# Kernel optimization log

Measured on AMD Instinct MI355X. Metric: run time of the kernel, lower is better.

## Reference

```python
import jax, jax.numpy as jnp
import numpy as np

NC = 32          # num context requests
NG = 32          # num generation requests
L = 4            # max_draft_len
CTX_LEN = 512    # tokens per context request
NCTX_TOK = NC * CTX_LEN            # 16384
NTOK = NCTX_TOK + NG * (L + 1)     # 16544
H = 2048
NCAP = 3                            # captured layers
VT = 50257                          # target vocab
VD = 32000                          # draft vocab


def setup_inputs() -> dict:
    key = jax.random.key(0)
    ks = jax.random.split(key, 10)
    logits = jax.random.normal(ks[0], (NC + NG * (L + 1), VT), jnp.float32)
    input_ids = jax.random.randint(ks[1], (NTOK,), 0, VT, jnp.int32)
    position_ids = jnp.arange(NTOK, dtype=jnp.int32)
    captured_hidden = jax.random.normal(ks[2], (NTOK, NCAP * H), jnp.float32)
    draft_tokens = jax.random.randint(ks[3], (NG * L,), 0, VT, jnp.int32)
    # last token index of each context request
    gather_ids_ctx = (jnp.arange(1, NC + 1, dtype=jnp.int32) * CTX_LEN - 1)
    s = 1.0 / np.sqrt(H)
    W_fc = jax.random.normal(ks[4], (NCAP * H, H), jnp.float32) * s
    embed = jax.random.normal(ks[5], (VT, H), jnp.float32) * s
    W_h = jax.random.normal(ks[6], (H, H), jnp.float32) * s
    lm_head = jax.random.normal(ks[7], (H, VD), jnp.float32) * s
    d2t = jax.random.randint(ks[8], (VD,), 0, VT - VD, jnp.int32)
    return {
        'logits': logits, 'input_ids': input_ids, 'position_ids': position_ids,
        'captured_hidden': captured_hidden, 'draft_tokens': draft_tokens,
        'gather_ids_ctx': gather_ids_ctx, 'W_fc': W_fc, 'embed': embed,
        'W_h': W_h, 'lm_head': lm_head, 'd2t': d2t,
        'num_contexts': NC, 'num_gens': NG, 'max_draft_len': L,
        'num_ctx_tokens': NCTX_TOK,
    }


def reference(logits, input_ids, position_ids, captured_hidden, draft_tokens,
              gather_ids_ctx, W_fc, embed, W_h, lm_head, d2t,
              num_contexts, num_gens, max_draft_len, num_ctx_tokens):
    nc, ng, l = num_contexts, num_gens, max_draft_len
    bsz = nc + ng

    # ---- sample_and_accept_draft_tokens ----
    target_tokens = jnp.argmax(logits, axis=-1).astype(jnp.int32)      # [nc + ng*(l+1)]
    gen_targets = target_tokens[nc:].reshape(ng, l + 1)
    acc_ctx = jnp.zeros((nc, l + 1), jnp.int32).at[:, 0].set(target_tokens[:nc])
    accepted = jnp.concatenate([acc_ctx, gen_targets], axis=0)          # [bsz, l+1]
    dt = draft_tokens.reshape(ng, l)
    matches = jnp.cumprod((dt == gen_targets[:, :l]).astype(jnp.int32), axis=-1).sum(-1)
    num_accepted = jnp.concatenate(
        [jnp.ones(nc, jnp.int32), (1 + matches).astype(jnp.int32)])     # [bsz]

    # ---- prepare_1st_drafter_inputs ----
    hidden = captured_hidden @ W_fc                                      # [T, H] eagle3 fc
    ctx_ids = input_ids[:num_ctx_tokens]
    ids_ctx = jnp.concatenate([ctx_ids[1:], jnp.zeros((1,), ctx_ids.dtype)])
    ids_ctx = ids_ctx.at[gather_ids_ctx].set(accepted[:nc, 0])
    ids = jnp.concatenate([ids_ctx.astype(jnp.int32), accepted[nc:].reshape(-1)])
    pos = position_ids

    # ---- draft loop ----
    next_draft = []
    for i in range(l):
        if i == 0:
            g_gen = (jnp.arange(ng, dtype=jnp.int32) * (l + 1)
                     + num_accepted[nc:] - 1 + num_ctx_tokens)
            gather = jnp.concatenate([gather_ids_ctx.astype(jnp.int32), g_gen])
        else:
            gather = jnp.arange(bsz, dtype=jnp.int32)
        h_new = jnp.tanh(embed[ids] + hidden @ W_h)                      # draft model step
        logits_d = h_new[gather] @ lm_head                               # [bsz, VD]
        tok = jnp.argmax(logits_d, axis=-1)
        tok = (d2t[tok] + tok).astype(jnp.int32)                         # draft->target vocab
        next_draft.append(tok)
        hidden = h_new[gather]
        pos = pos[gather] + 1
        ids = tok

    next_draft_tokens = jnp.stack(next_draft, axis=1)                    # [bsz, l]
    last_acc = accepted[jnp.arange(bsz), num_accepted - 1][:, None]
    next_new_tokens = jnp.concatenate([last_acc, next_draft_tokens], axis=1)
    return (logits, accepted, num_accepted, next_draft_tokens, next_new_tokens)
```

## Files before the change

### kernel.cpp

```cpp
#include <hip/hip_runtime.h>
#include <math.h>

#define VTOK 50257
#define VDRAFT 32000
#define HDIM 2048
#define TK 32

__global__ __launch_bounds__(256) void k_logits_argmax_copy(
    const float* __restrict__ logits, float* __restrict__ out, int* __restrict__ tgt)
{
  const int row = blockIdx.x;
  const size_t base = (size_t)row * VTOK;
  const float* src = logits + base;
  float* dst = out + base;
  const int tid = threadIdx.x;
  float best = -INFINITY; int bi = 0;
  for (int j = tid; j < VTOK; j += 256) {
    float v = src[j];
    dst[j] = v;
    if (v > best) { best = v; bi = j; }
  }
  __shared__ float sv[256];
  __shared__ int   si[256];
  sv[tid] = best; si[tid] = bi;
  __syncthreads();
  for (int s = 128; s > 0; s >>= 1) {
    if (tid < s) {
      float v = sv[tid + s]; int ix = si[tid + s];
      if (v > sv[tid] || (v == sv[tid] && ix < si[tid])) { sv[tid] = v; si[tid] = ix; }
    }
    __syncthreads();
  }
  if (tid == 0) tgt[row] = si[0];
}

__global__ void k_setup(const int* __restrict__ t, const int* __restrict__ draft,
                        const int* __restrict__ gctx,
                        float* __restrict__ out_acc, float* __restrict__ out_na,
                        float* __restrict__ out_next, int* __restrict__ ids_sel,
                        int* __restrict__ gidx)
{
  const int r = threadIdx.x;
  if (r >= 64) return;
  if (r < 32) {
    int tok = t[r];
    out_acc[r*5+0] = (float)tok;
    out_acc[r*5+1] = 0.f; out_acc[r*5+2] = 0.f; out_acc[r*5+3] = 0.f; out_acc[r*5+4] = 0.f;
    out_na[r] = 1.f;
    out_next[r*5+0] = (float)tok;
    ids_sel[r] = tok;
    gidx[r] = gctx[r];
  } else {
    int g = r - 32;
    int base = 32 + 5*g;
    int m = 0; bool ok = true;
    #pragma unroll
    for (int j = 0; j < 4; j++) {
      int tt = t[base + j];
      out_acc[r*5+j] = (float)tt;
      if (ok && draft[4*g + j] == tt) m++; else ok = false;
    }
    out_acc[r*5+4] = (float)t[base + 4];
    int na = 1 + m;
    out_na[r] = (float)na;
    int last = t[base + na - 1];
    out_next[r*5+0] = (float)last;
    ids_sel[r] = last;
    gidx[r] = 16384 + 5*g + na - 1;
  }
}

template<int ARGMAX>
__global__ __launch_bounds__(256) void k_gemm64(
    const float* __restrict__ A, const int* __restrict__ rowmap, int lda,
    const float* __restrict__ B, int ldb, int kchunk,
    float* __restrict__ P, int Pstride,
    float* __restrict__ pval, int* __restrict__ pidx)
{
  const int tid = threadIdx.x;
  const int j0 = blockIdx.x * 64;
  const int k0 = blockIdx.y * kchunk;
  const int tr = tid & 15;
  const int tc = tid >> 4;

  __shared__ float sA[TK * 66];
  __shared__ float sB[TK * 64];

  float acc[4][4];
  #pragma unroll
  for (int i = 0; i < 4; i++)
    #pragma unroll
    for (int j = 0; j < 4; j++) acc[i][j] = 0.f;

  const int arow = tid >> 2;
  const int kseg = (tid & 3) * 8;
  const int asrc = rowmap ? rowmap[arow] : arow;
  const float* Ap = A + (size_t)asrc * lda + k0 + kseg;

  const int bk = tid >> 3;
  const int bj = (tid & 7) * 8;
  const float* Bp = B + (size_t)(k0 + bk) * ldb + j0 + bj;

  for (int kb = 0; kb < kchunk; kb += TK) {
    float4 a0 = *(const float4*)(Ap);
    float4 a1 = *(const float4*)(Ap + 4);
    float4 b0 = *(const float4*)(Bp);
    float4 b1 = *(const float4*)(Bp + 4);
    Ap += TK;
    Bp += (size_t)TK * ldb;
    __syncthreads();
    sA[(kseg+0)*66 + arow] = a0.x;
    sA[(kseg+1)*66 + arow] = a0.y;
    sA[(kseg+2)*66 + arow] = a0.z;
    sA[(kseg+3)*66 + arow] = a0.w;
    sA[(kseg+4)*66 + arow] = a1.x;
    sA[(kseg+5)*66 + arow] = a1.y;
    sA[(kseg+6)*66 + arow] = a1.z;
    sA[(kseg+7)*66 + arow] = a1.w;
    *(float4*)&sB[bk*64 + bj]     = b0;
    *(float4*)&sB[bk*64 + bj + 4] = b1;
    __syncthreads();
    #pragma unroll
    for (int kk = 0; kk < TK; kk++) {
      float2 a01 = *(const float2*)&sA[kk*66 + tr*4];
      float2 a23 = *(const float2*)&sA[kk*66 + tr*4 + 2];
      float4 bv  = *(const float4*)&sB[kk*64 + tc*4];
      float av[4] = {a01.x, a01.y, a23.x, a23.y};
      float bw[4] = {bv.x, bv.y, bv.z, bv.w};
      #pragma unroll
      for (int i = 0; i < 4; i++)
        #pragma unroll
        for (int j = 0; j < 4; j++)
          acc[i][j] = fmaf(av[i], bw[j], acc[i][j]);
    }
  }

  if (ARGMAX == 0) {
    float* Pd = P + (size_t)blockIdx.y * 64 * Pstride;
    #pragma unroll
    for (int i = 0; i < 4; i++) {
      float4 v = make_float4(acc[i][0], acc[i][1], acc[i][2], acc[i][3]);
      *(float4*)&Pd[(size_t)(tr*4 + i) * Pstride + j0 + tc*4] = v;
    }
  } else {
    __syncthreads();
    float* rv = sA;
    int*   ri = (int*)sB;
    #pragma unroll
    for (int i = 0; i < 4; i++) {
      float b_ = acc[i][0]; int x_ = j0 + tc*4;
      #pragma unroll
      for (int j = 1; j < 4; j++)
        if (acc[i][j] > b_) { b_ = acc[i][j]; x_ = j0 + tc*4 + j; }
      rv[(tr*4 + i) * 16 + tc] = b_;
      ri[(tr*4 + i) * 16 + tc] = x_;
    }
    __syncthreads();
    if (tid < 64) {
      const int r = tid;
      float b_ = rv[r*16]; int x_ = ri[r*16];
      #pragma unroll 4
      for (int c = 1; c < 16; c++) {
        float v = rv[r*16 + c]; int ix = ri[r*16 + c];
        if (v > b_ || (v == b_ && ix < x_)) { b_ = v; x_ = ix; }
      }
      pval[(size_t)blockIdx.x * 64 + r] = b_;
      pidx[(size_t)blockIdx.x * 64 + r] = x_;
    }
  }
}

__global__ __launch_bounds__(256) void k_reduce4(const float* __restrict__ P, float* __restrict__ outb)
{
  const int i = blockIdx.x * 256 + threadIdx.x;
  const float4* p = (const float4*)P;
  float4 s  = p[i];
  float4 t1 = p[i + 32768];
  float4 t2 = p[i + 65536];
  float4 t3 = p[i + 98304];
  s.x += t1.x + t2.x + t3.x;
  s.y += t1.y + t2.y + t3.y;
  s.z += t1.z + t2.z + t3.z;
  s.w += t1.w + t2.w + t3.w;
  ((float4*)outb)[i] = s;
}

__global__ __launch_bounds__(256) void k_reduce4_tanh(
    const float* __restrict__ P, const float* __restrict__ embed,
    const int* __restrict__ ids, float* __restrict__ outb)
{
  const int i = blockIdx.x * 256 + threadIdx.x;
  const int r  = i >> 9;
  const int c4 = i & 511;
  const float4* p = (const float4*)P;
  float4 s  = p[i];
  float4 t1 = p[i + 32768];
  float4 t2 = p[i + 65536];
  float4 t3 = p[i + 98304];
  const float4 e = *(const float4*)(embed + (size_t)ids[r] * HDIM + c4*4);
  float4 o;
  o.x = tanhf(e.x + (s.x + t1.x + t2.x + t3.x));
  o.y = tanhf(e.y + (s.y + t1.y + t2.y + t3.y));
  o.z = tanhf(e.z + (s.z + t1.z + t2.z + t3.z));
  o.w = tanhf(e.w + (s.w + t1.w + t2.w + t3.w));
  ((float4*)outb)[i] = o;
}

__global__ void k_finalize(const float* __restrict__ pval, const int* __restrict__ pidx,
                           const int* __restrict__ d2t,
                           float* __restrict__ out_draft, float* __restrict__ out_next,
                           int* __restrict__ ids, int iter)
{
  const int r = threadIdx.x;
  float b_ = pval[r]; int x_ = pidx[r];
  for (int b = 1; b < 500; b++) {
    float v = pval[b*64 + r]; int ix = pidx[b*64 + r];
    if (v > b_ || (v == b_ && ix < x_)) { b_ = v; x_ = ix; }
  }
  int tok = d2t[x_] + x_;
  out_draft[r*4 + iter]     = (float)tok;
  out_next[r*5 + iter + 1]  = (float)tok;
  ids[r] = tok;
}

extern "C" void kernel_launch(void* const* d_in, const int* in_sizes, int n_in,
                              void* d_out, int out_size, void* d_ws, size_t ws_size,
                              hipStream_t stream)
{
  const float* logits = (const float*)d_in[0];
  const float* cap    = (const float*)d_in[3];
  const int*   draft  = (const int*)d_in[4];
  const int*   gctx   = (const int*)d_in[5];
  const float* Wfc    = (const float*)d_in[6];
  const float* embed  = (const float*)d_in[7];
  const float* Wh     = (const float*)d_in[8];
  const float* lmh    = (const float*)d_in[9];
  const int*   d2t    = (const int*)d_in[10];
  float* out = (float*)d_out;

  char* wsb = (char*)d_ws;
  int*   t_ws    = (int*)(wsb + 0);
  int*   ids_ws  = (int*)(wsb + 1024);
  int*   gidx_ws = (int*)(wsb + 1536);
  float* pval    = (float*)(wsb + 4096);
  int*   pidx    = (int*)(wsb + 4096 + 128000);
  float* P       = (float*)(wsb + 262144);
  float* hA      = (float*)(wsb + 262144 + 2097152);
  float* hB      = (float*)(wsb + 262144 + 2097152 + 524288);

  const size_t O1 = 9649344;
  const size_t O2 = 9649664;
  const size_t O3 = 9649728;
  const size_t O4 = 9649984;

  k_logits_argmax_copy<<<192, 256, 0, stream>>>(logits, out, t_ws);
  k_setup<<<1, 64, 0, stream>>>(t_ws, draft, gctx, out + O1, out + O2, out + O4, ids_ws, gidx_ws);

  k_gemm64<0><<<dim3(32, 4), 256, 0, stream>>>(cap, gidx_ws, 6144, Wfc, 2048, 1536, P, 2048, nullptr, nullptr);
  k_reduce4<<<128, 256, 0, stream>>>(P, hA);

  float* bufs[2] = {hA, hB};
  const float* cur = hA;
  for (int i = 0; i < 4; i++) {
    float* nxt = bufs[(i + 1) & 1];
    k_gemm64<0><<<dim3(32, 4), 256, 0, stream>>>(cur, nullptr, HDIM, Wh, HDIM, 512, P, HDIM, nullptr, nullptr);
    k_reduce4_tanh<<<128, 256, 0, stream>>>(P, embed, ids_ws, nxt);
    k_gemm64<1><<<dim3(500, 1), 256, 0, stream>>>(nxt, nullptr, HDIM, lmh, VDRAFT, 2048, nullptr, 0, pval, pidx);
    k_finalize<<<1, 64, 0, stream>>>(pval, pidx, d2t, out + O3, out + O4, ids_ws, i);
    cur = nxt;
  }
}
```

Measured before the change: 2.254 ms.

## Use split-bf16 MFMA for draft lm_head GEMM with fused argmax

Replaces the FP32 SIMT lm_head GEMM with a matrix-core kernel. The activations and weights are split into high and low bf16 parts, and three MFMA products are summed to approximate FP32 accuracy. The reduce/tanh kernel now also writes the bf16 hi/lo activations, while lm_head weights are converted to bf16 on the fly into double-buffered LDS. The aim is to cut the compute time of the 64x2048x32000 GEMM four times per step, at the cost of extra conversion work and a small risk of argmax ties flipping.

New measurement: 1.930 ms. 14.4% less time.

```diff
diff --git a/kernel.cpp b/kernel.cpp
--- a/kernel.cpp
+++ b/kernel.cpp
@@ -5,6 +5,18 @@
 #define VDRAFT 32000
 #define HDIM 2048
 #define TK 32
+
+typedef __attribute__((ext_vector_type(8))) short bf16x8;
+typedef __attribute__((ext_vector_type(4))) float f32x4;
+
+__device__ __forceinline__ short f2bf(float x) {
+  unsigned u = __float_as_uint(x);
+  unsigned r = (u + 0x7fffu + ((u >> 16) & 1u)) >> 16;
+  return (short)r;
+}
+__device__ __forceinline__ float bf2f(short s) {
+  return __uint_as_float(((unsigned)(unsigned short)s) << 16);
+}
 
 __global__ __launch_bounds__(256) void k_logits_argmax_copy(
     const float* __restrict__ logits, float* __restrict__ out, int* __restrict__ tgt)
@@ -187,7 +199,8 @@
 
 __global__ __launch_bounds__(256) void k_reduce4_tanh(
     const float* __restrict__ P, const float* __restrict__ embed,
-    const int* __restrict__ ids, float* __restrict__ outb)
+    const int* __restrict__ ids, float* __restrict__ outb,
+    short* __restrict__ Ahi, short* __restrict__ Alo)
 {
   const int i = blockIdx.x * 256 + threadIdx.x;
   const int r  = i >> 9;
@@ -204,6 +217,105 @@
   o.z = tanhf(e.z + (s.z + t1.z + t2.z + t3.z));
   o.w = tanhf(e.w + (s.w + t1.w + t2.w + t3.w));
   ((float4*)outb)[i] = o;
+  short4 h, l;
+  h.x = f2bf(o.x); l.x = f2bf(o.x - bf2f(h.x));
+  h.y = f2bf(o.y); l.y = f2bf(o.y - bf2f(h.y));
+  h.z = f2bf(o.z); l.z = f2bf(o.z - bf2f(h.z));
+  h.w = f2bf(o.w); l.w = f2bf(o.w - bf2f(h.w));
+  *(short4*)&Ahi[i*4] = h;
+  *(short4*)&Alo[i*4] = l;
+}
+
+__global__ __launch_bounds__(256) void k_lm_mfma(
+    const short* __restrict__ Ahi, const short* __restrict__ Alo,
+    const float* __restrict__ B,
+    float* __restrict__ pval, int* __restrict__ pidx)
+{
+  const int tid  = threadIdx.x;
+  const int lane = tid & 63;
+  const int w    = tid >> 6;
+  const int j0   = blockIdx.x * 64;
+
+  __shared__ short sBh[2][64 * 40];
+  __shared__ short sBl[2][64 * 40];
+
+  const int sdst = lane * 40 + w * 8;
+
+  const short* Aph = Ahi + (((w << 4) + (lane & 15)) * 2048) + ((lane >> 4) << 3);
+  const short* Apl = Alo + (((w << 4) + (lane & 15)) * 2048) + ((lane >> 4) << 3);
+  const int bro = (lane & 15) * 40 + ((lane >> 4) << 3);
+
+  f32x4 acc[4];
+  #pragma unroll
+  for (int cb = 0; cb < 4; cb++) acc[cb] = (f32x4){0.f, 0.f, 0.f, 0.f};
+
+  const float* Bp = B + (size_t)(w * 8) * VDRAFT + j0 + lane;
+
+  {
+    bf16x8 hv, lv;
+    #pragma unroll
+    for (int u = 0; u < 8; u++) {
+      float v = Bp[(size_t)u * VDRAFT];
+      short h = f2bf(v);
+      hv[u] = h; lv[u] = f2bf(v - bf2f(h));
+    }
+    *(bf16x8*)&sBh[0][sdst] = hv;
+    *(bf16x8*)&sBl[0][sdst] = lv;
+  }
+  Bp += (size_t)32 * VDRAFT;
+
+  for (int kt = 0; kt < 64; kt++) {
+    const int p = kt & 1;
+    float nv[8];
+    if (kt < 63) {
+      #pragma unroll
+      for (int u = 0; u < 8; u++) nv[u] = Bp[(size_t)u * VDRAFT];
+      Bp += (size_t)32 * VDRAFT;
+    }
+    bf16x8 ah = *(const bf16x8*)(Aph + kt * 32);
+    bf16x8 al = *(const bf16x8*)(Apl + kt * 32);
+    __syncthreads();
+    #pragma unroll
+    for (int cb = 0; cb < 4; cb++) {
+      bf16x8 bh = *(const bf16x8*)&sBh[p][cb * 640 + bro];
+      bf16x8 bl = *(const bf16x8*)&sBl[p][cb * 640 + bro];
+      acc[cb] = __builtin_amdgcn_mfma_f32_16x16x32_bf16(ah, bh, acc[cb], 0, 0, 0);
+      acc[cb] = __builtin_amdgcn_mfma_f32_16x16x32_bf16(ah, bl, acc[cb], 0, 0, 0);
+      acc[cb] = __builtin_amdgcn_mfma_f32_16x16x32_bf16(al, bh, acc[cb], 0, 0, 0);
+    }
+    if (kt < 63) {
+      bf16x8 hv, lv;
+      #pragma unroll
+      for (int u = 0; u < 8; u++) {
+        short h = f2bf(nv[u]);
+        hv[u] = h; lv[u] = f2bf(nv[u] - bf2f(h));
+      }
+      *(bf16x8*)&sBh[p ^ 1][sdst] = hv;
+      *(bf16x8*)&sBl[p ^ 1][sdst] = lv;
+    }
+  }
+
+  const int colbase = j0 + (lane & 15);
+  #pragma unroll
+  for (int r = 0; r < 4; r++) {
+    float bv = acc[0][r]; int bc = colbase;
+    #pragma unroll
+    for (int cb = 1; cb < 4; cb++) {
+      float v2 = acc[cb][r]; int c2 = colbase + 16*cb;
+      if (v2 > bv) { bv = v2; bc = c2; }
+    }
+    #pragma unroll
+    for (int m = 1; m < 16; m <<= 1) {
+      float ov = __shfl_xor(bv, m);
+      int   oc = __shfl_xor(bc, m);
+      if (ov > bv || (ov == bv && oc < bc)) { bv = ov; bc = oc; }
+    }
+    if ((lane & 15) == 0) {
+      int row = (w << 4) + ((lane >> 4) << 2) + r;
+      pval[(size_t)blockIdx.x * 64 + row] = bv;
+      pidx[(size_t)blockIdx.x * 64 + row] = bc;
+    }
+  }
 }
 
 __global__ void k_finalize(const float* __restrict__ pval, const int* __restrict__ pidx,
@@ -247,6 +359,8 @@
   float* P       = (float*)(wsb + 262144);
   float* hA      = (float*)(wsb + 262144 + 2097152);
   float* hB      = (float*)(wsb + 262144 + 2097152 + 524288);
+  short* Ahi     = (short*)(wsb + 3407872);
+  short* Alo     = (short*)(wsb + 3670016);
 
   const size_t O1 = 9649344;
   const size_t O2 = 9649664;
@@ -264,8 +378,8 @@
   for (int i = 0; i < 4; i++) {
     float* nxt = bufs[(i + 1) & 1];
     k_gemm64<0><<<dim3(32, 4), 256, 0, stream>>>(cur, nullptr, HDIM, Wh, HDIM, 512, P, HDIM, nullptr, nullptr);
-    k_reduce4_tanh<<<128, 256, 0, stream>>>(P, embed, ids_ws, nxt);
-    k_gemm64<1><<<dim3(500, 1), 256, 0, stream>>>(nxt, nullptr, HDIM, lmh, VDRAFT, 2048, nullptr, 0, pval, pidx);
+    k_reduce4_tanh<<<128, 256, 0, stream>>>(P, embed, ids_ws, nxt, Ahi, Alo);
+    k_lm_mfma<<<500, 256, 0, stream>>>(Ahi, Alo, lmh, pval, pidx);
     k_finalize<<<1, 64, 0, stream>>>(pval, pidx, d2t, out + O3, out + O4, ids_ws, i);
     cur = nxt;
   }
```
